# Performance work log

Measured on AMD Instinct MI355X. Metric: run time of the kernel, lower is better.

The kernel has to match this reference:

```python
import jax, jax.numpy as jnp
import numpy as np

T = 0.04
PIC_NUM = 4  # images per identity (hardcoded in SP_loss)


def setup_inputs() -> dict:
    key = jax.random.key(0)
    N, D = 8192, 256  # 2048 identities x 4 images, 256-dim ReID features
    x = jax.random.normal(key, (N, D), dtype=jnp.float32)
    x = x / jnp.linalg.norm(x, axis=1, keepdims=True)  # L2-normalize (cosine sims)
    return {"x": x}


def reference(x):
    N = x.shape[0]
    G = N // PIC_NUM  # number of identity groups
    s = (x @ x.T) / T  # [N, N] scaled similarity matrix

    # Diagonal 4x4 blocks: within-class similarities. [G, 4, 4]
    d4 = s.reshape(G, PIC_NUM, G, PIC_NUM)
    gidx = jnp.arange(G)
    pos = d4[gidx, :, gidx, :]  # [G, 4, 4]

    # hard positive: -T * log( sum_{i,j in class} exp(-dot_ij / T) )  (soft-min)
    hard_pos = -T * jax.nn.logsumexp(-pos.reshape(G, PIC_NUM * PIC_NUM), axis=1)

    # least-hard positive: T * log( sum_i 1 / (sum_j exp(-dot_ij / T)) )
    lse_row = jax.nn.logsumexp(-pos, axis=2)           # [G, 4] = log sum_j exp(-dot/T)
    least_pos = T * jax.nn.logsumexp(-lse_row, axis=1)  # [G]

    # negatives: T * log( sum_{i in class, j not in class} exp(dot_ij / T) )
    col_group = jnp.arange(N) // PIC_NUM              # [N]
    same = col_group[None, :] == gidx[:, None]        # [G, N] same-class column mask
    s3 = s.reshape(G, PIC_NUM, N)
    neg_masked = jnp.where(same[:, None, :], -jnp.inf, s3)
    neg = T * jax.nn.logsumexp(neg_masked.reshape(G, PIC_NUM * N), axis=1)  # [G]

    # Original detaches all three S vectors before forming the loss.
    hard_pos = jax.lax.stop_gradient(hard_pos)
    least_pos = jax.lax.stop_gradient(least_pos)
    neg = jax.lax.stop_gradient(neg)

    # alpha: harmonic mean of (hard, least-hard) when hard >= 0, else 0
    alpha = jnp.where(hard_pos >= 0.0,
                      2.0 * least_pos * hard_pos / (hard_pos + least_pos),
                      0.0)
    margin = alpha * hard_pos + (1.0 - alpha) * least_pos
    # log(1 + exp(z)) == softplus(z), numerically stable, same math
    loss = jnp.mean(jax.nn.softplus((neg - margin) / T))
    return loss
```

## Files before the change

### kernel.cpp

```cpp
#include <hip/hip_runtime.h>
#include <math.h>


#define NROWS 8192
#define DDIM  256
#define NGRP  2048
#define NTB   128
#define NTILES (NTB * (NTB + 1) / 2)
#define TPW   4
#define NWG   (NTILES / TPW)
#define T_CONST 0.04f
#define INV_T   25.0f
#define QSCALE  6.005612043932249f
#define SCALE_ONE 0x7F7F7F7Fu

typedef __attribute__((ext_vector_type(8))) int   i32x8_t;
typedef __attribute__((ext_vector_type(4))) int   i32x4_t;
typedef __attribute__((ext_vector_type(4))) float f32x4_t;

__device__ __forceinline__ i32x8_t ldfrag(const unsigned char* base, int off) {
    i32x4_t lo = *(const i32x4_t*)(base + off);
    i32x4_t hi = *(const i32x4_t*)(base + off + 16);
    return __builtin_shufflevector(lo, hi, 0, 1, 2, 3, 4, 5, 6, 7);
}

__global__ __launch_bounds__(256) void prep_kernel(const float* __restrict__ x,
                                                   unsigned int* __restrict__ xq,
                                                   float* __restrict__ grpsum,
                                                   float* __restrict__ margin) {
    const int b = blockIdx.x;
    if (b < 512) {
#pragma unroll
        for (int it = 0; it < 4; ++it) {
            int gid = it * 131072 + b * 256 + threadIdx.x;
            float4 v = *(const float4*)(x + (size_t)gid * 4);
            int pk = __builtin_amdgcn_cvt_pk_fp8_f32(v.x * QSCALE, v.y * QSCALE, 0, false);
            pk = __builtin_amdgcn_cvt_pk_fp8_f32(v.z * QSCALE, v.w * QSCALE, pk, true);
            xq[gid] = (unsigned int)pk;
            if (it == 0 && gid < NGRP) grpsum[gid] = 0.f;
        }
        return;
    }
    const int g = (b - 512) * 4 + (threadIdx.x >> 6);
    const int lane = threadIdx.x & 63;
    const float* xr = x + (size_t)g * 4 * DDIM;
    float a[16];
#pragma unroll
    for (int k = 0; k < 16; ++k) a[k] = 0.f;
    for (int e = lane; e < DDIM; e += 64) {
        float vv[4];
        vv[0] = xr[e];
        vv[1] = xr[DDIM + e];
        vv[2] = xr[2 * DDIM + e];
        vv[3] = xr[3 * DDIM + e];
#pragma unroll
        for (int i = 0; i < 4; ++i)
#pragma unroll
            for (int j = 0; j < 4; ++j)
                a[i * 4 + j] = fmaf(vv[i], vv[j], a[i * 4 + j]);
    }
#pragma unroll
    for (int k = 0; k < 16; ++k) {
        float t = a[k];
        t += __shfl_xor(t, 32, 64);
        t += __shfl_xor(t, 16, 64);
        t += __shfl_xor(t, 8, 64);
        t += __shfl_xor(t, 4, 64);
        t += __shfl_xor(t, 2, 64);
        t += __shfl_xor(t, 1, 64);
        a[k] = t;
    }
    if (lane == 0) {
        float pos[16];
#pragma unroll
        for (int k = 0; k < 16; ++k) pos[k] = a[k] * INV_T;

        float mx = -pos[0];
#pragma unroll
        for (int k = 1; k < 16; ++k) mx = fmaxf(mx, -pos[k]);
        float se = 0.f;
#pragma unroll
        for (int k = 0; k < 16; ++k) se += __expf(-pos[k] - mx);
        float hard_pos = -T_CONST * (mx + __logf(se));

        float lse_row[4];
#pragma unroll
        for (int i = 0; i < 4; ++i) {
            float m2 = -pos[i * 4];
#pragma unroll
            for (int j = 1; j < 4; ++j) m2 = fmaxf(m2, -pos[i * 4 + j]);
            float s2 = 0.f;
#pragma unroll
            for (int j = 0; j < 4; ++j) s2 += __expf(-pos[i * 4 + j] - m2);
            lse_row[i] = m2 + __logf(s2);
        }
        float m3 = -lse_row[0];
#pragma unroll
        for (int i = 1; i < 4; ++i) m3 = fmaxf(m3, -lse_row[i]);
        float s3 = 0.f;
#pragma unroll
        for (int i = 0; i < 4; ++i) s3 += __expf(-lse_row[i] - m3);
        float least_pos = T_CONST * (m3 + __logf(s3));

        float alpha = (hard_pos >= 0.f)
                          ? (2.f * least_pos * hard_pos) / (hard_pos + least_pos)
                          : 0.f;
        margin[g] = alpha * hard_pos + (1.f - alpha) * least_pos;
    }
}

__global__ __launch_bounds__(64, 2) void gemm_exp_grpsum(const unsigned char* __restrict__ xq,
                                                         float* __restrict__ grpsum) {
    const int idx0 = blockIdx.x * TPW;
    int ti = (int)((257.0f - sqrtf(66049.0f - 8.0f * (float)idx0)) * 0.5f);
    while (ti * (257 - ti) / 2 > idx0) --ti;
    while ((ti + 1) * (256 - ti) / 2 <= idx0) ++ti;
    int tj = ti + (idx0 - ti * (257 - ti) / 2);

    const int lane = threadIdx.x;
    const int quad = lane >> 4;
    const int l16 = lane & 15;

    int voff[8];
#pragma unroll
    for (int z = 0; z < 8; ++z)
        voff[z] = (((z & 3) * 16 + l16) << 8) + (z >> 2) * 128 + quad * 32;

    i32x8_t aF[2][4];
    int curTi = -1;

    i32x8_t bF[2][4];
    {
        const unsigned char* bb = xq + ((size_t)tj << 14);
#pragma unroll
        for (int z = 0; z < 8; ++z) bF[z >> 2][z & 3] = ldfrag(bb, voff[z]);
    }

#pragma unroll
    for (int t = 0; t < TPW; ++t) {
        const bool diag = (ti == tj);
        const int rg0 = ti * 16;
        const int cg0 = tj * 16;

        if (ti != curTi) {
            curTi = ti;
            const unsigned char* ab = xq + ((size_t)ti << 14);
#pragma unroll
            for (int z = 0; z < 8; ++z) aF[z >> 2][z & 3] = ldfrag(ab, voff[z]);
        }

        f32x4_t acc[4][4];
#pragma unroll
        for (int i = 0; i < 4; ++i)
#pragma unroll
            for (int j = 0; j < 4; ++j)
                acc[i][j] = (f32x4_t){0.f, 0.f, 0.f, 0.f};

#pragma unroll
        for (int ks = 0; ks < 2; ++ks)
#pragma unroll
            for (int mi = 0; mi < 4; ++mi)
#pragma unroll
                for (int ni = 0; ni < 4; ++ni)
                    acc[mi][ni] = __builtin_amdgcn_mfma_scale_f32_16x16x128_f8f6f4(
                        aF[ks][mi], bF[ks][ni], acc[mi][ni],
                        0, 0,
                        0, (int)SCALE_ONE,
                        0, (int)SCALE_ONE);

        const int ptj = tj;  (void)ptj;
        ++tj;
        if (tj == NTB) { ++ti; tj = ti; }
        if (t + 1 < TPW) {
            const unsigned char* bb = xq + ((size_t)tj << 14);
#pragma unroll
            for (int z = 0; z < 8; ++z) bF[z >> 2][z & 3] = ldfrag(bb, voff[z]);
        }

        float rowg[4] = {0.f, 0.f, 0.f, 0.f};
        float colp[4] = {0.f, 0.f, 0.f, 0.f};

        if (!diag) {
#pragma unroll
            for (int mi = 0; mi < 4; ++mi)
#pragma unroll
                for (int ni = 0; ni < 4; ++ni) {
                    float s4 = exp2f(acc[mi][ni][0]) + exp2f(acc[mi][ni][1])
                             + exp2f(acc[mi][ni][2]) + exp2f(acc[mi][ni][3]);
                    rowg[mi] += s4;
                    colp[ni] += s4;
                }
        } else {
#pragma unroll
            for (int mi = 0; mi < 4; ++mi) {
                const int rgrp = mi * 4 + quad;
#pragma unroll
                for (int ni = 0; ni < 4; ++ni) {
                    const int cgrp = ni * 4 + (l16 >> 2);
                    if (cgrp != rgrp) {
                        float s4 = exp2f(acc[mi][ni][0]) + exp2f(acc[mi][ni][1])
                                 + exp2f(acc[mi][ni][2]) + exp2f(acc[mi][ni][3]);
                        rowg[mi] += s4;
                    }
                }
            }
        }

#pragma unroll
        for (int mi = 0; mi < 4; ++mi) {
            float v = rowg[mi];
            v += __shfl_xor(v, 1, 64);
            v += __shfl_xor(v, 2, 64);
            v += __shfl_xor(v, 4, 64);
            v += __shfl_xor(v, 8, 64);
            if (l16 == 0) atomicAdd(&grpsum[rg0 + mi * 4 + quad], v);
        }
        if (!diag) {
#pragma unroll
            for (int ni = 0; ni < 4; ++ni) {
                float v = colp[ni];
                v += __shfl_xor(v, 16, 64);
                v += __shfl_xor(v, 32, 64);
                v += __shfl_xor(v, 1, 64);
                v += __shfl_xor(v, 2, 64);
                if (quad == 0 && (l16 & 3) == 0)
                    atomicAdd(&grpsum[cg0 + ni * 4 + (l16 >> 2)], v);
            }
        }
    }
}

__global__ __launch_bounds__(256) void finalize_kernel(const float* __restrict__ grpsum,
                                                       const float* __restrict__ margin,
                                                       float* __restrict__ out) {
    const int tid = threadIdx.x;
    float local = 0.f;
    for (int g = tid; g < NGRP; g += 256) {
        float z = __logf(grpsum[g]) - margin[g] * INV_T;
        float sp = (z > 30.f) ? z : log1pf(__expf(z));
        local += sp;
    }
    local += __shfl_xor(local, 1, 64);
    local += __shfl_xor(local, 2, 64);
    local += __shfl_xor(local, 4, 64);
    local += __shfl_xor(local, 8, 64);
    local += __shfl_xor(local, 16, 64);
    local += __shfl_xor(local, 32, 64);
    __shared__ float wsum[4];
    if ((tid & 63) == 0) wsum[tid >> 6] = local;
    __syncthreads();
    if (tid == 0) out[0] = (wsum[0] + wsum[1] + wsum[2] + wsum[3]) * (1.f / (float)NGRP);
}

extern "C" void kernel_launch(void* const* d_in, const int* in_sizes, int n_in,
                              void* d_out, int out_size, void* d_ws, size_t ws_size,
                              hipStream_t stream) {
    const float* x = (const float*)d_in[0];
    float* out = (float*)d_out;

    unsigned int* xq = (unsigned int*)d_ws;
    float* grpsum = (float*)((char*)d_ws + (size_t)NROWS * DDIM);
    float* margin = grpsum + NGRP;

    prep_kernel<<<1024, 256, 0, stream>>>(x, xq, grpsum, margin);
    gemm_exp_grpsum<<<NWG, 64, 0, stream>>>((const unsigned char*)xq, grpsum);
    finalize_kernel<<<1, 256, 0, stream>>>(grpsum, margin, out);
}
```

Before: 109.9 us.

## Replace grpsum atomics with per-tile partial buffer reduced in finalize

```diff
diff --git a/kernel.cpp b/kernel.cpp
--- a/kernel.cpp
+++ b/kernel.cpp
@@ -26,7 +26,6 @@
 
 __global__ __launch_bounds__(256) void prep_kernel(const float* __restrict__ x,
                                                    unsigned int* __restrict__ xq,
-                                                   float* __restrict__ grpsum,
                                                    float* __restrict__ margin) {
     const int b = blockIdx.x;
     if (b < 512) {
@@ -37,7 +36,6 @@
             int pk = __builtin_amdgcn_cvt_pk_fp8_f32(v.x * QSCALE, v.y * QSCALE, 0, false);
             pk = __builtin_amdgcn_cvt_pk_fp8_f32(v.z * QSCALE, v.w * QSCALE, pk, true);
             xq[gid] = (unsigned int)pk;
-            if (it == 0 && gid < NGRP) grpsum[gid] = 0.f;
         }
         return;
     }
@@ -109,8 +107,8 @@
     }
 }
 
-__global__ __launch_bounds__(64, 2) void gemm_exp_grpsum(const unsigned char* __restrict__ xq,
-                                                         float* __restrict__ grpsum) {
+__global__ __launch_bounds__(64) void gemm_exp_contrib(const unsigned char* __restrict__ xq,
+                                                       float* __restrict__ contrib) {
     const int idx0 = blockIdx.x * TPW;
     int ti = (int)((257.0f - sqrtf(66049.0f - 8.0f * (float)idx0)) * 0.5f);
     while (ti * (257 - ti) / 2 > idx0) --ti;
@@ -129,18 +127,8 @@
     i32x8_t aF[2][4];
     int curTi = -1;
 
-    i32x8_t bF[2][4];
-    {
-        const unsigned char* bb = xq + ((size_t)tj << 14);
-#pragma unroll
-        for (int z = 0; z < 8; ++z) bF[z >> 2][z & 3] = ldfrag(bb, voff[z]);
-    }
-
-#pragma unroll
     for (int t = 0; t < TPW; ++t) {
         const bool diag = (ti == tj);
-        const int rg0 = ti * 16;
-        const int cg0 = tj * 16;
 
         if (ti != curTi) {
             curTi = ti;
@@ -156,25 +144,21 @@
             for (int j = 0; j < 4; ++j)
                 acc[i][j] = (f32x4_t){0.f, 0.f, 0.f, 0.f};
 
-#pragma unroll
-        for (int ks = 0; ks < 2; ++ks)
+        const unsigned char* bb = xq + ((size_t)tj << 14);
+#pragma unroll
+        for (int ks = 0; ks < 2; ++ks) {
+            i32x8_t bF[4];
+#pragma unroll
+            for (int ni = 0; ni < 4; ++ni) bF[ni] = ldfrag(bb, voff[ks * 4 + ni]);
 #pragma unroll
             for (int mi = 0; mi < 4; ++mi)
 #pragma unroll
                 for (int ni = 0; ni < 4; ++ni)
                     acc[mi][ni] = __builtin_amdgcn_mfma_scale_f32_16x16x128_f8f6f4(
-                        aF[ks][mi], bF[ks][ni], acc[mi][ni],
+                        aF[ks][mi], bF[ni], acc[mi][ni],
                         0, 0,
                         0, (int)SCALE_ONE,
                         0, (int)SCALE_ONE);
-
-        const int ptj = tj;  (void)ptj;
-        ++tj;
-        if (tj == NTB) { ++ti; tj = ti; }
-        if (t + 1 < TPW) {
-            const unsigned char* bb = xq + ((size_t)tj << 14);
-#pragma unroll
-            for (int z = 0; z < 8; ++z) bF[z >> 2][z & 3] = ldfrag(bb, voff[z]);
         }
 
         float rowg[4] = {0.f, 0.f, 0.f, 0.f};
@@ -206,6 +190,7 @@
             }
         }
 
+        float* crow = contrib + (((size_t)ti * NTB + tj) << 4);
 #pragma unroll
         for (int mi = 0; mi < 4; ++mi) {
             float v = rowg[mi];
@@ -213,9 +198,10 @@
             v += __shfl_xor(v, 2, 64);
             v += __shfl_xor(v, 4, 64);
             v += __shfl_xor(v, 8, 64);
-            if (l16 == 0) atomicAdd(&grpsum[rg0 + mi * 4 + quad], v);
+            if (l16 == 0) crow[mi * 4 + quad] = v;
         }
         if (!diag) {
+            float* ccol = contrib + (((size_t)tj * NTB + ti) << 4);
 #pragma unroll
             for (int ni = 0; ni < 4; ++ni) {
                 float v = colp[ni];
@@ -223,22 +209,30 @@
                 v += __shfl_xor(v, 32, 64);
                 v += __shfl_xor(v, 1, 64);
                 v += __shfl_xor(v, 2, 64);
-                if (quad == 0 && (l16 & 3) == 0)
-                    atomicAdd(&grpsum[cg0 + ni * 4 + (l16 >> 2)], v);
+                if (quad == 0 && (l16 & 3) == 0) ccol[ni * 4 + (l16 >> 2)] = v;
             }
         }
-    }
-}
-
-__global__ __launch_bounds__(256) void finalize_kernel(const float* __restrict__ grpsum,
+
+        ++tj;
+        if (tj == NTB) { ++ti; tj = ti; }
+    }
+}
+
+__global__ __launch_bounds__(256) void finalize_kernel(const float* __restrict__ contrib,
                                                        const float* __restrict__ margin,
                                                        float* __restrict__ out) {
     const int tid = threadIdx.x;
     float local = 0.f;
-    for (int g = tid; g < NGRP; g += 256) {
-        float z = __logf(grpsum[g]) - margin[g] * INV_T;
-        float sp = (z > 30.f) ? z : log1pf(__expf(z));
-        local += sp;
+#pragma unroll
+    for (int k = 0; k < 8; ++k) {
+        const int g = tid + k * 256;
+        const int p = g >> 4;
+        const int idx = g & 15;
+        const float* base = contrib + (((size_t)p * NTB) << 4) + idx;
+        float s = 0.f;
+        for (int q = 0; q < NTB; ++q) s += base[q << 4];
+        float z = __logf(s) - margin[g] * INV_T;
+        local += (z > 30.f) ? z : log1pf(__expf(z));
     }
     local += __shfl_xor(local, 1, 64);
     local += __shfl_xor(local, 2, 64);
@@ -259,10 +253,10 @@
     float* out = (float*)d_out;
 
     unsigned int* xq = (unsigned int*)d_ws;
-    float* grpsum = (float*)((char*)d_ws + (size_t)NROWS * DDIM);
-    float* margin = grpsum + NGRP;
-
-    prep_kernel<<<1024, 256, 0, stream>>>(x, xq, grpsum, margin);
-    gemm_exp_grpsum<<<NWG, 64, 0, stream>>>((const unsigned char*)xq, grpsum);
-    finalize_kernel<<<1, 256, 0, stream>>>(grpsum, margin, out);
-}
+    float* contrib = (float*)((char*)d_ws + (size_t)NROWS * DDIM);
+    float* margin = contrib + (size_t)NTB * NTB * 16;
+
+    prep_kernel<<<1024, 256, 0, stream>>>(x, xq, margin);
+    gemm_exp_contrib<<<NWG, 64, 0, stream>>>((const unsigned char*)xq, contrib);
+    finalize_kernel<<<1, 256, 0, stream>>>(contrib, margin, out);
+}
```

After: 132.2 us. 20.4% more time.
